# Kernel optimization log

Measured on AMD Instinct MI355X. Metric: run time of the kernel, lower is better.

The kernel has to match this reference:

```python
import jax, jax.numpy as jnp
import numpy as np

B, S, E = 4, 2048, 1024
H = E // 2  # per-head dim (2 heads)


def setup_inputs() -> dict:
    key = jax.random.key(0)
    ks = jax.random.split(key, 10)
    w = 0.02
    return {
        "input": jax.random.normal(ks[0], (B, S, E), dtype=jnp.float32),
        "Wq": jax.random.normal(ks[1], (2, H, H), dtype=jnp.float32) * w,
        "bq": jax.random.normal(ks[2], (2, H), dtype=jnp.float32) * w,
        "Wk": jax.random.normal(ks[3], (2, H, H), dtype=jnp.float32) * w,
        "bk": jax.random.normal(ks[4], (2, H), dtype=jnp.float32) * w,
        "Wv": jax.random.normal(ks[5], (2, H, H), dtype=jnp.float32) * w,
        "bv": jax.random.normal(ks[6], (2, H), dtype=jnp.float32) * w,
        "Wf": jax.random.normal(ks[7], (E, E), dtype=jnp.float32) * w,
        "bf": jax.random.normal(ks[8], (E,), dtype=jnp.float32) * w,
        "masked": 1,
    }


def reference(input, Wq, bq, Wk, bk, Wv, bv, Wf, bf, masked):
    b, s, e = input.shape
    h = e // 2
    # contiguous split into 2 heads: [b, s, 2, h]
    xh = input.reshape(b, s, 2, h)
    # per-head Linear: y = x @ W.T + b  (W is [out, in])
    q = jnp.einsum("bsnh,noh->bsno", xh, Wq) + bq
    k = jnp.einsum("bsnh,noh->bsno", xh, Wk) + bk
    v = jnp.einsum("bsnh,noh->bsno", xh, Wv) + bv
    # scores: [b, n, s, t]
    scores = jnp.einsum("bsno,btno->bnst", q, k) / jnp.sqrt(jnp.float32(h))
    if masked:
        causal = jnp.tril(jnp.ones((s, s), dtype=bool))
        scores = jnp.where(causal, scores, jnp.float32(-jnp.inf))
    probs = jax.nn.softmax(scores, axis=-1)
    out = jnp.einsum("bnst,btnh->bsnh", probs, v).reshape(b, s, e)
    return jnp.einsum("bse,oe->bso", out, Wf) + bf
```

## Files before the change

kernel.cpp:

```cpp
#include <hip/hip_runtime.h>
#include <hip/hip_bf16.h>

#define BB 4
#define SS 2048
#define EE 1024
#define HH 512

typedef __attribute__((ext_vector_type(8))) short short8;
typedef __attribute__((ext_vector_type(4))) float f32x4;
typedef __attribute__((ext_vector_type(16))) float f32x16;
typedef __attribute__((ext_vector_type(4))) unsigned short us4;

static __device__ __forceinline__ unsigned short f2bf(float x){
  unsigned u = __float_as_uint(x);
  u += 0x7fffu + ((u >> 16) & 1u);
  return (unsigned short)(u >> 16);
}

static __device__ __forceinline__ unsigned cvtpk(float lo, float hi){
  unsigned d;
  asm("v_cvt_pk_bf16_f32 %0, %1, %2" : "=v"(d) : "v"(lo), "v"(hi));
  return d;
}

static __device__ __forceinline__ void gload16(const void* g, void* l){
  __builtin_amdgcn_global_load_lds((const __attribute__((address_space(1))) void*)g,
                                   (__attribute__((address_space(3))) void*)l, 16, 0, 0);
}

__global__ void k_cvt_all(const float* __restrict__ x,  const float* __restrict__ wq,
                          const float* __restrict__ wk, const float* __restrict__ wv,
                          const float* __restrict__ wf,
                          unsigned short* __restrict__ xb,  unsigned short* __restrict__ wqb,
                          unsigned short* __restrict__ wkb, unsigned short* __restrict__ wvb,
                          unsigned short* __restrict__ wfb){
  const int N0 = 1048576;
  const int N1 = N0 + 65536;
  const int N2 = N1 + 65536;
  const int N3 = N2 + 65536;
  const int N4 = N3 + 131072;
  int idx = blockIdx.x * blockDim.x + threadIdx.x;
  int stride = gridDim.x * blockDim.x;
  for (int i = idx; i < N4; i += stride){
    const float* src; unsigned short* dst; int j;
    if (i < N0){ src = x;  dst = xb;  j = i; }
    else if (i < N1){ src = wq; dst = wqb; j = i - N0; }
    else if (i < N2){ src = wk; dst = wkb; j = i - N1; }
    else if (i < N3){ src = wv; dst = wvb; j = i - N2; }
    else            { src = wf; dst = wfb; j = i - N3; }
    const float4* p = (const float4*)src + (long)j * 2;
    float4 a = p[0], b = p[1];
    union { unsigned short u[8]; uint4 v; } r;
    r.u[0]=f2bf(a.x); r.u[1]=f2bf(a.y); r.u[2]=f2bf(a.z); r.u[3]=f2bf(a.w);
    r.u[4]=f2bf(b.x); r.u[5]=f2bf(b.y); r.u[6]=f2bf(b.z); r.u[7]=f2bf(b.w);
    ((uint4*)dst)[j] = r.v;
  }
}

#define GBK 32

template<int OUTMODE>
static __device__ __forceinline__ void gemm_tile(
    const unsigned short* __restrict__ A, int lda,
    const unsigned short* __restrict__ Bw, int ldb,
    void* __restrict__ Cc, int ldc,
    const float* __restrict__ bias, int K, int row0, int col0, float oscale)
{
  __shared__ unsigned short As[2][128 * GBK];
  __shared__ unsigned short Bs[2][128 * GBK];
  const int tid = threadIdx.x, lane = tid & 63, w = tid >> 6;
  const int wm = w >> 1, wn = w & 1;
  const int fr = lane & 15, g = lane >> 4;

  f32x4 acc[4][4];
  #pragma unroll
  for (int i = 0; i < 4; i++)
    #pragma unroll
    for (int j = 0; j < 4; j++){ acc[i][j][0]=0.f; acc[i][j][1]=0.f; acc[i][j][2]=0.f; acc[i][j][3]=0.f; }

  const unsigned short* gAsrc[2]; const unsigned short* gBsrc[2];
  unsigned ldsOff[2];
  #pragma unroll
  for (int i = 0; i < 2; i++){
    int slot = w*128 + i*64 + lane;
    int row = slot >> 2, ch = slot & 3;
    int sc_ = ch ^ ((row >> 1) & 3);
    gAsrc[i] = A  + (long)(row0 + row) * lda + sc_ * 8;
    gBsrc[i] = Bw + (long)(col0 + row) * ldb + sc_ * 8;
    ldsOff[i] = (unsigned)((w*128 + i*64) * 8);
  }

  unsigned aoff[4], boff[4];
  #pragma unroll
  for (int mi = 0; mi < 4; mi++){
    int row = wm*64 + mi*16 + fr;
    aoff[mi] = row * GBK + ((g ^ ((row >> 1) & 3)) * 8);
  }
  #pragma unroll
  for (int ni = 0; ni < 4; ni++){
    int row = wn*64 + ni*16 + fr;
    boff[ni] = row * GBK + ((g ^ ((row >> 1) & 3)) * 8);
  }

  const int KT = K / GBK;
  #pragma unroll
  for (int i = 0; i < 2; i++) gload16(gAsrc[i], &As[0][ldsOff[i]]);
  #pragma unroll
  for (int i = 0; i < 2; i++) gload16(gBsrc[i], &Bs[0][ldsOff[i]]);
  __syncthreads();

  for (int kt = 0; kt < KT; ++kt){
    const int cur = kt & 1;
    if (kt + 1 < KT){
      #pragma unroll
      for (int i = 0; i < 2; i++) gload16(gAsrc[i] + (kt+1)*GBK, &As[cur^1][ldsOff[i]]);
      #pragma unroll
      for (int i = 0; i < 2; i++) gload16(gBsrc[i] + (kt+1)*GBK, &Bs[cur^1][ldsOff[i]]);
    }
    short8 av[4], bv[4];
    #pragma unroll
    for (int mi = 0; mi < 4; mi++) av[mi] = *(const short8*)&As[cur][aoff[mi]];
    #pragma unroll
    for (int ni = 0; ni < 4; ni++) bv[ni] = *(const short8*)&Bs[cur][boff[ni]];
    #pragma unroll
    for (int mi = 0; mi < 4; mi++)
      #pragma unroll
      for (int ni = 0; ni < 4; ni++)
        acc[mi][ni] = __builtin_amdgcn_mfma_f32_16x16x32_bf16(av[mi], bv[ni], acc[mi][ni], 0, 0, 0);
    __syncthreads();
  }

  if constexpr (OUTMODE == 2){
    __shared__ unsigned short Ct[128][136];
    #pragma unroll
    for (int mi = 0; mi < 4; mi++){
      #pragma unroll
      for (int ni = 0; ni < 4; ni++){
        int rowb = wm*64 + mi*16 + g*4;
        int col  = wn*64 + ni*16 + fr;
        float bb = bias[col0 + col];
        us4 pk;
        #pragma unroll
        for (int r = 0; r < 4; r++) pk[r] = f2bf((acc[mi][ni][r] + bb) * oscale);
        *(us4*)&Ct[col][rowb] = pk;
      }
    }
    __syncthreads();
    #pragma unroll
    for (int it = 0; it < 8; it++){
      int idx2 = it * 256 + tid;
      int o = idx2 >> 4, sch = idx2 & 15;
      uint4 v = *(const uint4*)&Ct[o][sch * 8];
      *(uint4*)&((unsigned short*)Cc)[(long)(col0 + o) * ldc + row0 + sch * 8] = v;
    }
  } else {
    #pragma unroll
    for (int mi = 0; mi < 4; mi++){
      #pragma unroll
      for (int ni = 0; ni < 4; ni++){
        int row = row0 + wm*64 + mi*16 + g*4;
        int col = col0 + wn*64 + ni*16 + fr;
        float bb = bias[col];
        #pragma unroll
        for (int r = 0; r < 4; r++){
          float v = (acc[mi][ni][r] + bb) * oscale;
          if (OUTMODE == 1) ((unsigned short*)Cc)[(long)(row + r) * ldc + col] = f2bf(v);
          else              ((float*)Cc)[(long)(row + r) * ldc + col] = v;
        }
      }
    }
  }
}

__global__ __launch_bounds__(256, 2) void k_qkv(
    const unsigned short* __restrict__ xb,
    const unsigned short* __restrict__ wq, const unsigned short* __restrict__ wk,
    const float* __restrict__ bq, const float* __restrict__ bk,
    unsigned short* __restrict__ Q, unsigned short* __restrict__ K)
{
  int z = blockIdx.z; int which = z >> 3; int bn = z & 7; int b = bn >> 1, n = bn & 1;
  const unsigned short* W; const float* bias; unsigned short* out;
  float os = 1.f;
  if (which == 0){ W = wq; bias = bq; out = Q; os = 0.044194173824159216f; }
  else { W = wk; bias = bk; out = K; }
  W += n * HH * HH; bias += n * HH; out += (long)bn * SS * HH;
  const unsigned short* Ap = xb + (long)b * SS * EE + n * HH;
  gemm_tile<1>(Ap, EE, W, HH, out, HH, bias, HH, blockIdx.x * 128, blockIdx.y * 128, os);
}

__global__ __launch_bounds__(256, 2) void k_qkv_v(
    const unsigned short* __restrict__ xb, const unsigned short* __restrict__ wv,
    const float* __restrict__ bv, unsigned short* __restrict__ Vt)
{
  int bn = blockIdx.z; int b = bn >> 1, n = bn & 1;
  const unsigned short* W = wv + n * HH * HH;
  const float* bias = bv + n * HH;
  unsigned short* out = Vt + (long)bn * SS * HH;
  const unsigned short* Ap = xb + (long)b * SS * EE + n * HH;
  gemm_tile<2>(Ap, EE, W, HH, out, SS, bias, HH, blockIdx.x * 128, blockIdx.y * 128, 1.f);
}

__global__ __launch_bounds__(256, 2) void k_outproj(
    const unsigned short* __restrict__ O, const unsigned short* __restrict__ wf,
    const float* __restrict__ bfb, float* __restrict__ out)
{
  gemm_tile<0>(O, EE, wf, EE, out, EE, bfb, EE, blockIdx.x * 128, blockIdx.y * 128, 1.f);
}

#define QB 128
#define TB 32

__global__ __launch_bounds__(512, 1) void k_flash8(
    const unsigned short* __restrict__ Qg, const unsigned short* __restrict__ Kg,
    const unsigned short* __restrict__ Vtg,
    unsigned short* __restrict__ Opart, float* __restrict__ mlg,
    const int* __restrict__ maskedp)
{
  __shared__ unsigned short Ks[2][TB * HH];
  __shared__ unsigned short Vs[HH * TB];
  __shared__ float4 Sx[4][2][4][64];

  const int bid = blockIdx.x;
  const int bn = bid & 7;
  const int u = bid >> 3;
  const int masked = *maskedp;
  int qi, c;
  if (masked){
    qi = -1; c = 0;
    int cnt = 0;
    #pragma unroll 1
    for (int q = 0; q < 16; q++){
      int nch = (4*q + 25) / 22;
      if (qi < 0 && u >= cnt && u < cnt + nch){ qi = q; c = u - cnt; }
      cnt += nch;
    }
    if (qi < 0) return;
  } else { qi = u >> 1; c = u & 1; }
  const int n  = masked ? 4*qi + 4 : 64;
  const int CH = masked ? 22 : 32;
  const int t0 = c * CH;
  const int t1 = min(n, t0 + CH);

  const long base = (long)bn * SS * HH;
  const unsigned short* Qp = Qg + base;
  const unsigned short* Kp = Kg + base;
  const unsigned short* Vp = Vtg + base;

  const int tid = threadIdx.x, lane = tid & 63, w = tid >> 6;
  const int ln = lane & 31, hi = lane >> 5;
  const int rg = w & 3, dh = w >> 2;
  const int q0 = qi * QB;
  const int myq = q0 + rg * 32 + ln;

  short8 Qr[16];
  {
    const unsigned short* qrow = Qp + (long)myq * HH + dh * 256 + hi * 8;
    #pragma unroll
    for (int ks = 0; ks < 16; ks++) Qr[ks] = *(const short8*)(qrow + ks * 16);
  }

  f32x16 oa[8];
  #pragma unroll
  for (int i = 0; i < 8; i++)
    #pragma unroll
    for (int r = 0; r < 16; r++) oa[i][r] = 0.f;
  float m_r = -1e30f, l_r = 0.f;

  auto stageK = [&](int buf, int t){
    if (w < 4){
      #pragma unroll
      for (int i = 0; i < 8; i++){
        const int sbase = w * 512 + i * 64;
        const int slot = sbase + lane;
        int row = slot >> 6, ch = slot & 63;
        int sc_ = ch ^ (row & 7);
        gload16(Kp + (long)(t * TB + row) * HH + sc_ * 8, &Ks[buf][sbase * 8]);
      }
    }
  };
  auto stageV = [&](int t){
    if (w >= 4){
      #pragma unroll
      for (int i = 0; i < 8; i++){
        const int sbase = (w - 4) * 512 + i * 64;
        const int slot = sbase + lane;
        int row = slot >> 2, ch = slot & 3;
        int sc_ = ch ^ ((row >> 1) & 3);
        gload16(Vp + (long)row * SS + t * TB + sc_ * 8, &Vs[sbase * 8]);
      }
    }
  };

  stageK(0, t0);
  stageV(t0);
  __syncthreads();

  for (int t = t0; t < t1; ++t){
    const int cur = (t - t0) & 1;
    if (t > t0) stageV(t);

    f32x16 sa;
    #pragma unroll
    for (int r = 0; r < 16; r++) sa[r] = 0.f;
    #pragma unroll
    for (int ks = 0; ks < 16; ks++){
      int ch = (dh * 32 + ks * 2 + hi) ^ (ln & 7);
      short8 kf = *(const short8*)&Ks[cur][ln * HH + ch * 8];
      sa = __builtin_amdgcn_mfma_f32_32x32x16_bf16(kf, Qr[ks], sa, 0, 0, 0);
    }

    #pragma unroll
    for (int ip = 0; ip < 4; ip++)
      Sx[rg][dh][ip][lane] = make_float4(sa[4*ip], sa[4*ip+1], sa[4*ip+2], sa[4*ip+3]);

    __syncthreads();

    if (t + 1 < t1) stageK(cur ^ 1, t + 1);

    float p[16];
    #pragma unroll
    for (int ip = 0; ip < 4; ip++){
      float4 o = Sx[rg][dh ^ 1][ip][lane];
      p[4*ip]   = sa[4*ip]   + o.x;
      p[4*ip+1] = sa[4*ip+1] + o.y;
      p[4*ip+2] = sa[4*ip+2] + o.z;
      p[4*ip+3] = sa[4*ip+3] + o.w;
    }

    if (masked && (t * TB + TB - 1 > myq)){
      #pragma unroll
      for (int r = 0; r < 16; r++){
        int tl = (r & 3) + 8 * (r >> 2) + 4 * hi;
        if (t * TB + tl > myq) p[r] = -1e30f;
      }
    }

    float mx = p[0];
    #pragma unroll
    for (int r = 1; r < 16; r++) mx = fmaxf(mx, p[r]);
    mx = fmaxf(mx, __shfl_xor(mx, 32, 64));
    if (__any(mx > m_r + 8.f)){
      float mn = fmaxf(m_r, mx);
      float alpha = __expf(m_r - mn);
      m_r = mn; l_r *= alpha;
      #pragma unroll
      for (int r = 0; r < 16; r++){
        float al = __shfl(alpha, (r & 3) + 8 * (r >> 2) + 4 * hi, 64);
        #pragma unroll
        for (int i = 0; i < 8; i++) oa[i][r] *= al;
      }
    }
    float ps = 0.f;
    #pragma unroll
    for (int r = 0; r < 16; r++){ float pe = __expf(p[r] - m_r); p[r] = pe; ps += pe; }
    ps += __shfl_xor(ps, 32, 64);
    l_r += ps;

    unsigned W[8], R[8];
    #pragma unroll
    for (int i = 0; i < 8; i++) W[i] = cvtpk(p[2*i], p[2*i+1]);
    #pragma unroll
    for (int i = 0; i < 8; i++) R[i] = __shfl_xor(W[i], 32, 64);
    union { unsigned u[4]; short8 s; } fa0, fa1;
    fa0.u[0] = hi ? R[2] : W[0];  fa0.u[1] = hi ? R[3] : W[1];
    fa0.u[2] = hi ? W[2] : R[0];  fa0.u[3] = hi ? W[3] : R[1];
    fa1.u[0] = hi ? R[6] : W[4];  fa1.u[1] = hi ? R[7] : W[5];
    fa1.u[2] = hi ? W[6] : R[4];  fa1.u[3] = hi ? W[7] : R[5];

    #pragma unroll
    for (int cf = 0; cf < 8; cf++){
      int h = dh * 256 + cf * 32 + ln;
      int sw = (h >> 1) & 3;
      short8 v0 = *(const short8*)&Vs[h * TB + ((hi     ^ sw) * 8)];
      oa[cf] = __builtin_amdgcn_mfma_f32_32x32x16_bf16(fa0.s, v0, oa[cf], 0, 0, 0);
      short8 v1 = *(const short8*)&Vs[h * TB + (((2+hi) ^ sw) * 8)];
      oa[cf] = __builtin_amdgcn_mfma_f32_32x32x16_bf16(fa1.s, v1, oa[cf], 0, 0, 0);
    }

    __syncthreads();
  }

  const long slot = (long)(bn * 16 + qi) * 3 + c;
  unsigned short* dst = Opart + slot * (QB * HH);
  #pragma unroll
  for (int cf = 0; cf < 8; cf++){
    int col = dh * 256 + cf * 32 + ln;
    #pragma unroll
    for (int r = 0; r < 16; r++){
      int row = rg * 32 + (r & 3) + 8 * (r >> 2) + 4 * hi;
      dst[row * HH + col] = f2bf(oa[cf][r]);
    }
  }
  if (w < 4 && hi == 0){
    mlg[slot * 256 + rg * 32 + ln]       = m_r;
    mlg[slot * 256 + 128 + rg * 32 + ln] = l_r;
  }
}

__global__ __launch_bounds__(256) void k_combine(
    const unsigned short* __restrict__ Opart, const float* __restrict__ mlg,
    unsigned short* __restrict__ O, const int* __restrict__ maskedp)
{
  __shared__ float wl[128][3];
  const int gq = blockIdx.x;
  const int bn = gq & 7, qi = gq >> 3;
  const int b = bn >> 1, n = bn & 1;
  const int NC = (*maskedp) ? (4*qi + 25) / 22 : 2;
  const long slotbase = (long)(bn * 16 + qi) * 3;
  const int tid = threadIdx.x;

  if (tid < 128){
    float mc[3], lc[3];
    float M = -1e30f;
    for (int c = 0; c < NC; c++){
      mc[c] = mlg[(slotbase + c) * 256 + tid];
      lc[c] = mlg[(slotbase + c) * 256 + 128 + tid];
      M = fmaxf(M, mc[c]);
    }
    float L = 0.f;
    for (int c = 0; c < NC; c++){
      float wc = __expf(mc[c] - M);
      mc[c] = wc;
      L += lc[c] * wc;
    }
    float inv = 1.f / L;
    #pragma unroll
    for (int c = 0; c < 3; c++) wl[tid][c] = (c < NC) ? mc[c] * inv : 0.f;
  }
  __syncthreads();

  for (int it = 0; it < 32; it++){
    int idx = it * 256 + tid;
    int row = idx >> 6, cv = idx & 63;
    float acc[8] = {0.f,0.f,0.f,0.f,0.f,0.f,0.f,0.f};
    for (int c = 0; c < NC; c++){
      float wc = wl[row][c];
      short8 v = *(const short8*)&Opart[(slotbase + c) * (QB * HH) + row * HH + cv * 8];
      #pragma unroll
      for (int j = 0; j < 8; j++){
        float f = __uint_as_float((unsigned)(unsigned short)v[j] << 16);
        acc[j] += f * wc;
      }
    }
    union { unsigned short u[8]; uint4 q; } rr;
    #pragma unroll
    for (int j = 0; j < 8; j++) rr.u[j] = f2bf(acc[j]);
    long dstoff = ((long)b * SS + qi * QB + row) * EE + n * HH + cv * 8;
    *(uint4*)&O[dstoff] = rr.q;
  }
}

extern "C" void kernel_launch(void* const* d_in, const int* in_sizes, int n_in,
                              void* d_out, int out_size, void* d_ws, size_t ws_size,
                              hipStream_t stream)
{
  const float* x   = (const float*)d_in[0];
  const float* Wq  = (const float*)d_in[1];
  const float* bq  = (const float*)d_in[2];
  const float* Wk  = (const float*)d_in[3];
  const float* bk  = (const float*)d_in[4];
  const float* Wv  = (const float*)d_in[5];
  const float* bv  = (const float*)d_in[6];
  const float* Wf  = (const float*)d_in[7];
  const float* bf_ = (const float*)d_in[8];
  const int* masked = (const int*)d_in[9];

  char* p = (char*)d_ws;
  const long TEN = (long)BB * SS * EE * 2;
  unsigned short* xb  = (unsigned short*)p; p += TEN;
  unsigned short* Qb  = (unsigned short*)p; p += TEN;
  unsigned short* Kb  = (unsigned short*)p; p += TEN;
  unsigned short* Vt  = (unsigned short*)p; p += TEN;
  unsigned short* Ob  = (unsigned short*)p; p += TEN;
  unsigned short* wqb = (unsigned short*)p; p += 2L * HH * HH * 2;
  unsigned short* wkb = (unsigned short*)p; p += 2L * HH * HH * 2;
  unsigned short* wvb = (unsigned short*)p; p += 2L * HH * HH * 2;
  unsigned short* wfb = (unsigned short*)p; p += (long)EE * EE * 2;
  unsigned short* Opart = (unsigned short*)p; p += 384L * QB * HH * 2;
  float* mlg = (float*)p; p += 384L * 256 * 4;

  k_cvt_all<<<dim3(2048), 256, 0, stream>>>(x, Wq, Wk, Wv, Wf, xb, wqb, wkb, wvb, wfb);
  k_qkv   <<<dim3(SS / 128, HH / 128, 16), 256, 0, stream>>>(xb, wqb, wkb, bq, bk, Qb, Kb);
  k_qkv_v <<<dim3(SS / 128, HH / 128, 8),  256, 0, stream>>>(xb, wvb, bv, Vt);
  k_flash8<<<dim3(256), 512, 0, stream>>>(Qb, Kb, Vt, Opart, mlg, masked);
  k_combine<<<dim3(128), 256, 0, stream>>>(Opart, mlg, Ob, masked);
  k_outproj<<<dim3((BB * SS) / 128, EE / 128, 1), 256, 0, stream>>>(Ob, wfb, bf_, (float*)d_out);
}
```

Baseline: 265.3 us.

## Double-buffer V tiles and prefetch K/V next tile at loop start in flash kernel

Adds a second V shared-memory buffer so the next K and V tiles are both prefetched at the start of each iteration, overlapping the whole next-tile load with the QK, softmax and PV work. The mid-loop __syncthreads is replaced by an explicit lgkmcnt wait plus a raw s_barrier fenced by sched_barriers, and the score exchange buffer now uses float2 instead of float4. LDS use grows by another 32KB V buffer, and the raw barrier relies on vmcnt ordering being handled elsewhere for the async global-to-LDS loads.

After: 244.3 us. 1.09x faster.

```diff
diff --git a/kernel.cpp b/kernel.cpp
--- a/kernel.cpp
+++ b/kernel.cpp
@@ -210,15 +210,17 @@
 #define QB 128
 #define TB 32
 
-__global__ __launch_bounds__(512, 1) void k_flash8(
+#define LGKM0 asm volatile("s_waitcnt lgkmcnt(0)" ::: "memory")
+
+__global__ __launch_bounds__(512, 1) void k_flash9(
     const unsigned short* __restrict__ Qg, const unsigned short* __restrict__ Kg,
     const unsigned short* __restrict__ Vtg,
     unsigned short* __restrict__ Opart, float* __restrict__ mlg,
     const int* __restrict__ maskedp)
 {
   __shared__ unsigned short Ks[2][TB * HH];
-  __shared__ unsigned short Vs[HH * TB];
-  __shared__ float4 Sx[4][2][4][64];
+  __shared__ unsigned short Vs[2][HH * TB];
+  __shared__ float2 Sx[4][2][8][64];
 
   const int bid = blockIdx.x;
   const int bn = bid & 7;
@@ -278,7 +280,7 @@
       }
     }
   };
-  auto stageV = [&](int t){
+  auto stageV = [&](int buf, int t){
     if (w >= 4){
       #pragma unroll
       for (int i = 0; i < 8; i++){
@@ -286,18 +288,19 @@
         const int slot = sbase + lane;
         int row = slot >> 2, ch = slot & 3;
         int sc_ = ch ^ ((row >> 1) & 3);
-        gload16(Vp + (long)row * SS + t * TB + sc_ * 8, &Vs[sbase * 8]);
+        gload16(Vp + (long)row * SS + t * TB + sc_ * 8, &Vs[buf][sbase * 8]);
       }
     }
   };
 
   stageK(0, t0);
-  stageV(t0);
+  stageV(0, t0);
   __syncthreads();
 
   for (int t = t0; t < t1; ++t){
     const int cur = (t - t0) & 1;
-    if (t > t0) stageV(t);
+
+    if (t + 1 < t1){ stageK(cur ^ 1, t + 1); stageV(cur ^ 1, t + 1); }
 
     f32x16 sa;
     #pragma unroll
@@ -310,21 +313,20 @@
     }
 
     #pragma unroll
-    for (int ip = 0; ip < 4; ip++)
-      Sx[rg][dh][ip][lane] = make_float4(sa[4*ip], sa[4*ip+1], sa[4*ip+2], sa[4*ip+3]);
-
-    __syncthreads();
-
-    if (t + 1 < t1) stageK(cur ^ 1, t + 1);
+    for (int i = 0; i < 8; i++)
+      Sx[rg][dh][i][lane] = make_float2(sa[2*i], sa[2*i+1]);
+
+    LGKM0;
+    __builtin_amdgcn_sched_barrier(0);
+    __builtin_amdgcn_s_barrier();
+    __builtin_amdgcn_sched_barrier(0);
 
     float p[16];
     #pragma unroll
-    for (int ip = 0; ip < 4; ip++){
-      float4 o = Sx[rg][dh ^ 1][ip][lane];
-      p[4*ip]   = sa[4*ip]   + o.x;
-      p[4*ip+1] = sa[4*ip+1] + o.y;
-      p[4*ip+2] = sa[4*ip+2] + o.z;
-      p[4*ip+3] = sa[4*ip+3] + o.w;
+    for (int i = 0; i < 8; i++){
+      float2 o = Sx[rg][dh ^ 1][i][lane];
+      p[2*i]   = sa[2*i]   + o.x;
+      p[2*i+1] = sa[2*i+1] + o.y;
     }
 
     if (masked && (t * TB + TB - 1 > myq)){
@@ -371,9 +373,9 @@
     for (int cf = 0; cf < 8; cf++){
       int h = dh * 256 + cf * 32 + ln;
       int sw = (h >> 1) & 3;
-      short8 v0 = *(const short8*)&Vs[h * TB + ((hi     ^ sw) * 8)];
+      short8 v0 = *(const short8*)&Vs[cur][h * TB + ((hi     ^ sw) * 8)];
       oa[cf] = __builtin_amdgcn_mfma_f32_32x32x16_bf16(fa0.s, v0, oa[cf], 0, 0, 0);
-      short8 v1 = *(const short8*)&Vs[h * TB + (((2+hi) ^ sw) * 8)];
+      short8 v1 = *(const short8*)&Vs[cur][h * TB + (((2+hi) ^ sw) * 8)];
       oa[cf] = __builtin_amdgcn_mfma_f32_32x32x16_bf16(fa1.s, v1, oa[cf], 0, 0, 0);
     }
 
@@ -482,7 +484,7 @@
   k_cvt_all<<<dim3(2048), 256, 0, stream>>>(x, Wq, Wk, Wv, Wf, xb, wqb, wkb, wvb, wfb);
   k_qkv   <<<dim3(SS / 128, HH / 128, 16), 256, 0, stream>>>(xb, wqb, wkb, bq, bk, Qb, Kb);
   k_qkv_v <<<dim3(SS / 128, HH / 128, 8),  256, 0, stream>>>(xb, wvb, bv, Vt);
-  k_flash8<<<dim3(256), 512, 0, stream>>>(Qb, Kb, Vt, Opart, mlg, masked);
+  k_flash9<<<dim3(256), 512, 0, stream>>>(Qb, Kb, Vt, Opart, mlg, masked);
   k_combine<<<dim3(128), 256, 0, stream>>>(Opart, mlg, Ob, masked);
   k_outproj<<<dim3((BB * SS) / 128, EE / 128, 1), 256, 0, stream>>>(Ob, wfb, bf_, (float*)d_out);
 }
```
